# Optimization experiments

Hardware: AMD Instinct MI355X
Metric: run time of the kernel (lower is better)

The kernel has to match this reference:

```python
import jax, jax.numpy as jnp
import numpy as np

B, T, D, H, HD, L, V = 2048, 64, 128, 4, 32, 6, 256
DFF = 4 * D
PARAM_NAMES = ['tok_emb', 'pos_emb', 'Wq', 'Wk', 'Wv', 'Wo', 'bo', 'ln1_g', 'ln1_b',
               'W1', 'b1', 'W2', 'b2', 'ln2_g', 'ln2_b', 'lnf_g', 'lnf_b', 'Wh', 'bh']


def setup_inputs() -> dict:
    key = jax.random.key(0)
    ks = jax.random.split(key, 12)
    def n(k, shape, s=0.02):
        return jax.random.normal(k, shape, jnp.float32) * s
    return dict(
        idx=jax.random.randint(ks[0], (B, T), 0, V),
        tok_emb=n(ks[1], (V, D)),
        pos_emb=n(ks[2], (T, D)),
        Wq=n(ks[3], (L, H, D, HD)),
        Wk=n(ks[4], (L, H, D, HD)),
        Wv=n(ks[5], (L, H, D, HD)),
        Wo=n(ks[6], (L, D, D)), bo=jnp.zeros((L, D), jnp.float32),
        ln1_g=jnp.ones((L, D), jnp.float32), ln1_b=jnp.zeros((L, D), jnp.float32),
        W1=n(ks[7], (L, D, DFF)), b1=jnp.zeros((L, DFF), jnp.float32),
        W2=n(ks[8], (L, DFF, D)), b2=jnp.zeros((L, D), jnp.float32),
        ln2_g=jnp.ones((L, D), jnp.float32), ln2_b=jnp.zeros((L, D), jnp.float32),
        lnf_g=jnp.ones((D,), jnp.float32), lnf_b=jnp.zeros((D,), jnp.float32),
        Wh=n(ks[9], (D, V)), bh=jnp.zeros((V,), jnp.float32),
    )


def _ln(x, g, b):
    m = x.mean(-1, keepdims=True)
    v = x.var(-1, keepdims=True)  # biased, matches torch LayerNorm
    return (x - m) / jnp.sqrt(v + 1e-5) * g + b


def _forward(idx, p):
    x = p['tok_emb'][idx] + p['pos_emb'][None, :, :]  # [B,T,D]
    mask = jnp.tril(jnp.ones((T, T), bool))

    def block(x, lp):
        Wq, Wk, Wv, Wo, bo, g1, bb1, W1, b1, W2, b2, g2, bb2 = lp
        h = _ln(x, g1, bb1)
        q = jnp.einsum('btd,hde->bhte', h, Wq)
        k = jnp.einsum('btd,hde->bhte', h, Wk)
        v = jnp.einsum('btd,hde->bhte', h, Wv)
        s = jnp.einsum('bhte,bhse->bhts', q, k) * (HD ** -0.5)
        s = jnp.where(mask, s, -jnp.inf)
        w = jax.nn.softmax(s, axis=-1)  # dropout inactive (eval mode)
        o = jnp.einsum('bhts,bhse->bthe', w, v).reshape(B, T, D)  # concat heads
        x = x + o @ Wo + bo
        h2 = _ln(x, g2, bb2)
        x = x + jax.nn.relu(h2 @ W1 + b1) @ W2 + b2
        return x, None

    lp = (p['Wq'], p['Wk'], p['Wv'], p['Wo'], p['bo'], p['ln1_g'], p['ln1_b'],
          p['W1'], p['b1'], p['W2'], p['b2'], p['ln2_g'], p['ln2_b'])
    x, _ = jax.lax.scan(block, x, lp)
    x = _ln(x, p['lnf_g'], p['lnf_b'])
    return x @ p['Wh'] + p['bh']  # [B,T,V] logits


def reference(idx, tok_emb, pos_emb, Wq, Wk, Wv, Wo, bo, ln1_g, ln1_b,
              W1, b1, W2, b2, ln2_g, ln2_b, lnf_g, lnf_b, Wh, bh):
    p = dict(zip(PARAM_NAMES, (tok_emb, pos_emb, Wq, Wk, Wv, Wo, bo, ln1_g, ln1_b,
                               W1, b1, W2, b2, ln2_g, ln2_b, lnf_g, lnf_b, Wh, bh)))
    return _forward(idx, p)
```

## Files before the change

kernel.cpp:

```cpp
#include <hip/hip_runtime.h>

typedef unsigned short ushort_t;
typedef __attribute__((ext_vector_type(8))) short short8;
typedef __attribute__((ext_vector_type(4))) float float4_;

#define B_   2048
#define T_   64
#define D_   128
#define H_   4
#define HD_  32
#define L_   6
#define V_   256
#define DFF_ 512
#define BT_  (B_*T_)

static __device__ __forceinline__ float b2f(ushort_t u) {
    return __uint_as_float(((unsigned int)u) << 16);
}
static __device__ __forceinline__ ushort_t f2b(float f) {
    unsigned int x = __float_as_uint(f);
    return (ushort_t)((x + 0x7fffu + ((x >> 16) & 1u)) >> 16);
}
static __device__ __forceinline__ int bf16_mode(const ushort_t* flag_src) {
    return flag_src[0] == 0x3F80;
}

#define AS1C(p) ((const __attribute__((address_space(1))) void*)(p))
#define AS3(p)  ((__attribute__((address_space(3))) void*)(p))

#define NCVT 19
struct Cvt {
    const void* src[NCVT];
    long base[NCVT];
    long total;
};

__global__ __launch_bounds__(256) void convert_all(
    Cvt c, ushort_t* __restrict__ dst, const ushort_t* __restrict__ flag_src)
{
    long i = (long)blockIdx.x * 256 + threadIdx.x;
    if (i >= c.total) return;
    int s = 0;
    #pragma unroll 1
    while (s + 1 < NCVT && i >= c.base[s + 1]) s++;
    long j = i - c.base[s];
    if (bf16_mode(flag_src))
        dst[i] = ((const ushort_t*)c.src[s])[j];
    else
        dst[i] = f2b(((const float*)c.src[s])[j]);
}

__global__ __launch_bounds__(256) void repack_qkv(
    const ushort_t* __restrict__ Wq, const ushort_t* __restrict__ Wk,
    const ushort_t* __restrict__ Wv, ushort_t* __restrict__ outw)
{
    int i = blockIdx.x * 256 + threadIdx.x;
    int d = i & 127;
    int c = (i >> 7) % 384;
    int l = i / (384 * 128);
    int sel = c >> 7, hh = (c >> 5) & 3, e = c & 31;
    const ushort_t* W = (sel == 0) ? Wq : (sel == 1) ? Wk : Wv;
    outw[i] = W[((l * 4 + hh) * 128 + d) * 32 + e];
}

__global__ __launch_bounds__(256) void transpose_w(
    const ushort_t* __restrict__ in, ushort_t* __restrict__ out, int K, int N)
{
    long i = (long)blockIdx.x * 256 + threadIdx.x;
    int n = (int)(i % N);
    int k = (int)((i / N) % K);
    int l = (int)(i / ((long)N * K));
    out[((long)l * N + n) * K + k] = in[i];
}

__global__ __launch_bounds__(256) void embed_ln_kernel(
    const int* __restrict__ idx, const ushort_t* __restrict__ tok,
    const ushort_t* __restrict__ pos, const ushort_t* __restrict__ g,
    const ushort_t* __restrict__ bta, float* __restrict__ x,
    ushort_t* __restrict__ hout)
{
    int row  = blockIdx.x * 4 + (threadIdx.x >> 6);
    int lane = threadIdx.x & 63;
    int t = row & 63;
    int id = idx[row];
    float v0 = b2f(tok[id * 128 + lane])      + b2f(pos[t * 128 + lane]);
    float v1 = b2f(tok[id * 128 + lane + 64]) + b2f(pos[t * 128 + lane + 64]);
    long o = (long)row * 128 + lane;
    x[o] = v0; x[o + 64] = v1;
    float s  = v0 + v1;
    float sq = v0 * v0 + v1 * v1;
    #pragma unroll
    for (int off = 1; off < 64; off <<= 1) {
        s  += __shfl_xor(s,  off);
        sq += __shfl_xor(sq, off);
    }
    float mean = s * (1.0f / 128.0f);
    float var  = sq * (1.0f / 128.0f) - mean * mean;
    float rstd = rsqrtf(var + 1e-5f);
    hout[o]      = f2b((v0 - mean) * rstd * b2f(g[lane])      + b2f(bta[lane]));
    hout[o + 64] = f2b((v1 - mean) * rstd * b2f(g[lane + 64]) + b2f(bta[lane + 64]));
}

__global__ __launch_bounds__(256) void gemm_bt(
    const ushort_t* __restrict__ A, const ushort_t* __restrict__ Bt,
    const ushort_t* __restrict__ bias, void* __restrict__ outp,
    const ushort_t* __restrict__ flag, int M, int N, int K, int relu)
{
    __shared__ __align__(16) ushort_t As[128 * 64];
    __shared__ __align__(16) ushort_t Bs[128 * 64];
    const int tid  = threadIdx.x;
    const int wave = tid >> 6, lane = tid & 63;
    const int wm = wave >> 1, wn = wave & 1;
    const int row0 = blockIdx.x * 128, col0 = blockIdx.y * 128;

    float4_ acc[4][4];
    #pragma unroll
    for (int m = 0; m < 4; m++)
        #pragma unroll
        for (int n = 0; n < 4; n++) acc[m][n] = (float4_)0.0f;

    const int srow = lane >> 3;
    const int scg  = (lane & 7) ^ srow;
    const int fr = lane & 15, fq = lane >> 4;

    for (int k0 = 0; k0 < K; k0 += 64) {
        __syncthreads();
        #pragma unroll
        for (int i = 0; i < 4; i++) {
            int chunk = wave * 4 + i;
            int r = chunk * 8 + srow;
            __builtin_amdgcn_global_load_lds(
                AS1C(&A[(size_t)(row0 + r) * K + k0 + scg * 8]),
                AS3(&As[chunk * 512]), 16, 0, 0);
            __builtin_amdgcn_global_load_lds(
                AS1C(&Bt[(size_t)(col0 + r) * K + k0 + scg * 8]),
                AS3(&Bs[chunk * 512]), 16, 0, 0);
        }
        __syncthreads();

        #pragma unroll
        for (int ks = 0; ks < 2; ks++) {
            short8 af[4], bf[4];
            #pragma unroll
            for (int mt = 0; mt < 4; mt++) {
                int r = wm * 64 + mt * 16 + fr;
                af[mt] = *(const short8*)&As[r * 64 + (((ks * 4 + fq) ^ (r & 7)) * 8)];
            }
            #pragma unroll
            for (int nt = 0; nt < 4; nt++) {
                int r = wn * 64 + nt * 16 + fr;
                bf[nt] = *(const short8*)&Bs[r * 64 + (((ks * 4 + fq) ^ (r & 7)) * 8)];
            }
            #pragma unroll
            for (int mt = 0; mt < 4; mt++)
                #pragma unroll
                for (int nt = 0; nt < 4; nt++)
                    acc[mt][nt] = __builtin_amdgcn_mfma_f32_16x16x32_bf16(
                        af[mt], bf[nt], acc[mt][nt], 0, 0, 0);
        }
    }

    const int out_bf16 = (flag == nullptr) || bf16_mode(flag);
    #pragma unroll
    for (int nt = 0; nt < 4; nt++) {
        int gcol = col0 + wn * 64 + nt * 16 + fr;
        float bb = bias ? b2f(bias[gcol]) : 0.0f;
        #pragma unroll
        for (int mt = 0; mt < 4; mt++) {
            #pragma unroll
            for (int i = 0; i < 4; i++) {
                int grow = row0 + wm * 64 + mt * 16 + fq * 4 + i;
                float v = acc[mt][nt][i] + bb;
                if (relu) v = fmaxf(v, 0.0f);
                long off = (long)grow * N + gcol;
                if (out_bf16) ((ushort_t*)outp)[off] = f2b(v);
                else          ((float*)outp)[off] = v;
            }
        }
    }
}

__global__ __launch_bounds__(256) void gemm_ln(
    const ushort_t* __restrict__ A, const ushort_t* __restrict__ Bt,
    const ushort_t* __restrict__ bias, float* __restrict__ x,
    const ushort_t* __restrict__ g, const ushort_t* __restrict__ bta,
    ushort_t* __restrict__ hout, int M, int K)
{
    __shared__ __align__(16) ushort_t As[128 * 64];
    __shared__ __align__(16) ushort_t Bs[128 * 64];
    __shared__ float stats[128][2][2];
    const int tid  = threadIdx.x;
    const int wave = tid >> 6, lane = tid & 63;
    const int wm = wave >> 1, wn = wave & 1;
    const int row0 = blockIdx.x * 128;
    const int N = 128;

    float4_ acc[4][4];
    #pragma unroll
    for (int m = 0; m < 4; m++)
        #pragma unroll
        for (int n = 0; n < 4; n++) acc[m][n] = (float4_)0.0f;

    const int srow = lane >> 3;
    const int scg  = (lane & 7) ^ srow;
    const int fr = lane & 15, fq = lane >> 4;

    for (int k0 = 0; k0 < K; k0 += 64) {
        __syncthreads();
        #pragma unroll
        for (int i = 0; i < 4; i++) {
            int chunk = wave * 4 + i;
            int r = chunk * 8 + srow;
            __builtin_amdgcn_global_load_lds(
                AS1C(&A[(size_t)(row0 + r) * K + k0 + scg * 8]),
                AS3(&As[chunk * 512]), 16, 0, 0);
            __builtin_amdgcn_global_load_lds(
                AS1C(&Bt[(size_t)r * K + k0 + scg * 8]),
                AS3(&Bs[chunk * 512]), 16, 0, 0);
        }
        __syncthreads();

        #pragma unroll
        for (int ks = 0; ks < 2; ks++) {
            short8 af[4], bf[4];
            #pragma unroll
            for (int mt = 0; mt < 4; mt++) {
                int r = wm * 64 + mt * 16 + fr;
                af[mt] = *(const short8*)&As[r * 64 + (((ks * 4 + fq) ^ (r & 7)) * 8)];
            }
            #pragma unroll
            for (int nt = 0; nt < 4; nt++) {
                int r = wn * 64 + nt * 16 + fr;
                bf[nt] = *(const short8*)&Bs[r * 64 + (((ks * 4 + fq) ^ (r & 7)) * 8)];
            }
            #pragma unroll
            for (int mt = 0; mt < 4; mt++)
                #pragma unroll
                for (int nt = 0; nt < 4; nt++)
                    acc[mt][nt] = __builtin_amdgcn_mfma_f32_16x16x32_bf16(
                        af[mt], bf[nt], acc[mt][nt], 0, 0, 0);
        }
    }

    int   col[4];
    float bbias[4], gg[4], bln[4];
    #pragma unroll
    for (int nt = 0; nt < 4; nt++) {
        col[nt]  = wn * 64 + nt * 16 + fr;
        bbias[nt] = b2f(bias[col[nt]]);
        gg[nt]    = b2f(g[col[nt]]);
        bln[nt]   = b2f(bta[col[nt]]);
    }
    #pragma unroll
    for (int mt = 0; mt < 4; mt++) {
        #pragma unroll
        for (int i = 0; i < 4; i++) {
            int lr = wm * 64 + mt * 16 + fq * 4 + i;
            long rbase = (long)(row0 + lr) * N;
            float s = 0.0f, sq = 0.0f;
            #pragma unroll
            for (int nt = 0; nt < 4; nt++) {
                float nx = x[rbase + col[nt]] + acc[mt][nt][i] + bbias[nt];
                x[rbase + col[nt]] = nx;
                acc[mt][nt][i] = nx;
                s += nx; sq += nx * nx;
            }
            s  += __shfl_xor(s, 1);  sq += __shfl_xor(sq, 1);
            s  += __shfl_xor(s, 2);  sq += __shfl_xor(sq, 2);
            s  += __shfl_xor(s, 4);  sq += __shfl_xor(sq, 4);
            s  += __shfl_xor(s, 8);  sq += __shfl_xor(sq, 8);
            if (fr == 0) { stats[lr][wn][0] = s; stats[lr][wn][1] = sq; }
        }
    }
    __syncthreads();
    #pragma unroll
    for (int mt = 0; mt < 4; mt++) {
        #pragma unroll
        for (int i = 0; i < 4; i++) {
            int lr = wm * 64 + mt * 16 + fq * 4 + i;
            float s  = stats[lr][0][0] + stats[lr][1][0];
            float sq = stats[lr][0][1] + stats[lr][1][1];
            float mean = s * (1.0f / 128.0f);
            float var  = sq * (1.0f / 128.0f) - mean * mean;
            float rstd = rsqrtf(var + 1e-5f);
            long rbase = (long)(row0 + lr) * N;
            #pragma unroll
            for (int nt = 0; nt < 4; nt++) {
                float nx = acc[mt][nt][i];
                hout[rbase + col[nt]] = f2b((nx - mean) * rstd * gg[nt] + bln[nt]);
            }
        }
    }
}

__global__ __launch_bounds__(256) void attn_kernel(
    const ushort_t* __restrict__ qkv,
    ushort_t* __restrict__ out)
{
    __shared__ __align__(16) ushort_t Qs[64][40];
    __shared__ __align__(16) ushort_t Ks[64][40];
    __shared__ __align__(16) ushort_t Vt[32][72];
    __shared__ __align__(16) ushort_t Pb[64][72];
    const int tid = threadIdx.x;
    const int b = blockIdx.x >> 2, h = blockIdx.x & 3;
    const long base = (long)b * T_ * 384 + h * 32;

    {
        int t = tid >> 2, e8 = (tid & 3) * 8;
        const ushort_t* p = &qkv[base + (long)t * 384 + e8];
        short8 qv = *(const short8*)(p);
        short8 kv = *(const short8*)(p + 128);
        short8 vv = *(const short8*)(p + 256);
        *(short8*)&Qs[t][e8] = qv;
        *(short8*)&Ks[t][e8] = kv;
        #pragma unroll
        for (int j = 0; j < 8; j++) Vt[e8 + j][t] = (ushort_t)vv[j];
    }
    __syncthreads();

    const int w = tid >> 6, lane = tid & 63, fr = lane & 15, fq = lane >> 4;

    short8 qf = *(const short8*)&Qs[w * 16 + fr][fq * 8];
    float4_ s[4];
    #pragma unroll
    for (int tj = 0; tj < 4; tj++) s[tj] = (float4_)0.0f;
    #pragma unroll
    for (int tj = 0; tj < 4; tj++) {
        if (tj <= w) {
            short8 kf = *(const short8*)&Ks[tj * 16 + fr][fq * 8];
            s[tj] = __builtin_amdgcn_mfma_f32_16x16x32_bf16(qf, kf, s[tj], 0, 0, 0);
        }
    }

    const float scale = 0.17677669529663687f;
    float pv[4][4];
    #pragma unroll
    for (int i = 0; i < 4; i++) {
        float mx = -1.0e30f;
        float vv4[4];
        int   ok[4];
        #pragma unroll
        for (int tj = 0; tj < 4; tj++) {
            ok[tj] = (tj < w) || (tj == w && fr <= fq * 4 + i);
            float v = ok[tj] ? s[tj][i] * scale : -1.0e30f;
            vv4[tj] = v;
            mx = fmaxf(mx, v);
        }
        mx = fmaxf(mx, __shfl_xor(mx, 1));
        mx = fmaxf(mx, __shfl_xor(mx, 2));
        mx = fmaxf(mx, __shfl_xor(mx, 4));
        mx = fmaxf(mx, __shfl_xor(mx, 8));
        float sm = 0.0f;
        #pragma unroll
        for (int tj = 0; tj < 4; tj++) {
            float e = ok[tj] ? __expf(vv4[tj] - mx) : 0.0f;
            vv4[tj] = e;
            sm += e;
        }
        sm += __shfl_xor(sm, 1);
        sm += __shfl_xor(sm, 2);
        sm += __shfl_xor(sm, 4);
        sm += __shfl_xor(sm, 8);
        float inv = 1.0f / sm;
        #pragma unroll
        for (int tj = 0; tj < 4; tj++) pv[i][tj] = vv4[tj] * inv;
    }
    #pragma unroll
    for (int tj = 0; tj < 4; tj++)
        #pragma unroll
        for (int i = 0; i < 4; i++)
            Pb[w * 16 + fq * 4 + i][tj * 16 + fr] = f2b(pv[i][tj]);
    __syncthreads();

    float4_ o[2];
    o[0] = (float4_)0.0f; o[1] = (float4_)0.0f;
    #pragma unroll
    for (int ks = 0; ks < 2; ks++) {
        short8 pf = *(const short8*)&Pb[w * 16 + fr][ks * 32 + fq * 8];
        #pragma unroll
        for (int nt = 0; nt < 2; nt++) {
            short8 vf = *(const short8*)&Vt[nt * 16 + fr][ks * 32 + fq * 8];
            o[nt] = __builtin_amdgcn_mfma_f32_16x16x32_bf16(pf, vf, o[nt], 0, 0, 0);
        }
    }
    #pragma unroll
    for (int nt = 0; nt < 2; nt++)
        #pragma unroll
        for (int i = 0; i < 4; i++)
            out[(long)(b * T_ + w * 16 + fq * 4 + i) * 128 + h * 32 + nt * 16 + fr]
                = f2b(o[nt][i]);
}

extern "C" void kernel_launch(void* const* d_in, const int* in_sizes, int n_in,
                              void* d_out, int out_size, void* d_ws, size_t ws_size,
                              hipStream_t stream)
{
    (void)in_sizes; (void)n_in; (void)out_size; (void)ws_size;
    const int* idx = (const int*)d_in[0];
    const ushort_t* flag = (const ushort_t*)d_in[8];

    char* ws = (char*)d_ws;
    float*    x    = (float*)ws;     ws += (size_t)BT_ * D_ * 4;
    ushort_t* h    = (ushort_t*)ws;  ws += (size_t)BT_ * D_ * 2;
    ushort_t* qkvb = (ushort_t*)ws;  ws += (size_t)BT_ * 384 * 2;
    ushort_t* ao   = (ushort_t*)ws;  ws += (size_t)BT_ * D_ * 2;
    ushort_t* mid  = qkvb;
    ushort_t* wqkv = (ushort_t*)ws;  ws += (size_t)L_ * 384 * 128 * 2;
    ushort_t* wo   = (ushort_t*)ws;  ws += (size_t)L_ * 128 * 128 * 2;
    ushort_t* w1   = (ushort_t*)ws;  ws += (size_t)L_ * 512 * 128 * 2;
    ushort_t* w2   = (ushort_t*)ws;  ws += (size_t)L_ * 128 * 512 * 2;
    ushort_t* wh   = (ushort_t*)ws;  ws += (size_t)256 * 128 * 2;
    ushort_t* cvt  = (ushort_t*)ws;

    static const long cnt[NCVT] = {
        (long)V_*D_, (long)T_*D_,
        (long)L_*H_*D_*HD_, (long)L_*H_*D_*HD_, (long)L_*H_*D_*HD_,
        (long)L_*D_*D_, (long)L_*D_,
        (long)L_*D_, (long)L_*D_,
        (long)L_*D_*DFF_, (long)L_*DFF_,
        (long)L_*DFF_*D_, (long)L_*D_,
        (long)L_*D_, (long)L_*D_,
        (long)D_, (long)D_,
        (long)D_*V_, (long)V_
    };
    Cvt c;
    long off = 0;
    for (int i = 0; i < NCVT; i++) { c.src[i] = d_in[i + 1]; c.base[i] = off; off += cnt[i]; }
    c.total = off;
    ushort_t* ctok  = cvt + c.base[0];
    ushort_t* cpos  = cvt + c.base[1];
    ushort_t* cWq   = cvt + c.base[2];
    ushort_t* cWk   = cvt + c.base[3];
    ushort_t* cWv   = cvt + c.base[4];
    ushort_t* cWo   = cvt + c.base[5];
    ushort_t* cbo   = cvt + c.base[6];
    ushort_t* cln1g = cvt + c.base[7];
    ushort_t* cln1b = cvt + c.base[8];
    ushort_t* cW1   = cvt + c.base[9];
    ushort_t* cb1   = cvt + c.base[10];
    ushort_t* cW2   = cvt + c.base[11];
    ushort_t* cb2   = cvt + c.base[12];
    ushort_t* cln2g = cvt + c.base[13];
    ushort_t* cln2b = cvt + c.base[14];
    ushort_t* clnfg = cvt + c.base[15];
    ushort_t* clnfb = cvt + c.base[16];
    ushort_t* cWh   = cvt + c.base[17];
    ushort_t* cbh   = cvt + c.base[18];

    convert_all<<<(int)((c.total + 255) / 256), 256, 0, stream>>>(c, cvt, flag);

    repack_qkv <<<1152, 256, 0, stream>>>(cWq, cWk, cWv, wqkv);
    transpose_w<<<384,  256, 0, stream>>>(cWo, wo, 128, 128);
    transpose_w<<<1536, 256, 0, stream>>>(cW1, w1, 128, 512);
    transpose_w<<<1536, 256, 0, stream>>>(cW2, w2, 512, 128);
    transpose_w<<<128,  256, 0, stream>>>(cWh, wh, 128, 256);
    embed_ln_kernel<<<BT_ / 4, 256, 0, stream>>>(idx, ctok, cpos, cln1g, cln1b, x, h);

    for (int l = 0; l < L_; l++) {
        gemm_bt<<<dim3(BT_ / 128, 3), 256, 0, stream>>>(
            h, wqkv + l * 384 * 128, nullptr, qkvb, nullptr, BT_, 384, 128, 0);
        attn_kernel<<<B_ * H_, 256, 0, stream>>>(qkvb, ao);
        gemm_ln<<<BT_ / 128, 256, 0, stream>>>(
            ao, wo + l * 128 * 128, cbo + l * 128, x,
            cln2g + l * 128, cln2b + l * 128, h, BT_, 128);
        gemm_bt<<<dim3(BT_ / 128, 4), 256, 0, stream>>>(
            h, w1 + l * 512 * 128, cb1 + l * 512, mid, nullptr, BT_, 512, 128, 1);
        const ushort_t* ng = (l < L_ - 1) ? (cln1g + (l + 1) * 128) : clnfg;
        const ushort_t* nb = (l < L_ - 1) ? (cln1b + (l + 1) * 128) : clnfb;
        gemm_ln<<<BT_ / 128, 256, 0, stream>>>(
            mid, w2 + l * 128 * 512, cb2 + l * 128, x, ng, nb, h, BT_, 512);
    }
    gemm_bt<<<dim3(BT_ / 128, 2), 256, 0, stream>>>(
        h, wh, cbh, d_out, flag, BT_, 256, 128, 0);
}
```

Measured before the change: 1.689 ms.

## Fuse FFN up-projection, ReLU and down-projection into one kernel

```diff
diff --git a/kernel.cpp b/kernel.cpp
--- a/kernel.cpp
+++ b/kernel.cpp
@@ -293,6 +293,195 @@
     }
 }
 
+__global__ __launch_bounds__(256) void ffn_fused(
+    const ushort_t* __restrict__ hin,
+    const ushort_t* __restrict__ w1,
+    const ushort_t* __restrict__ b1v,
+    const ushort_t* __restrict__ w2,
+    const ushort_t* __restrict__ b2v,
+    float* __restrict__ x,
+    const ushort_t* __restrict__ g, const ushort_t* __restrict__ bta,
+    ushort_t* __restrict__ hout)
+{
+    __shared__ __align__(16) ushort_t Hs[128 * 128];
+    __shared__ __align__(16) ushort_t Ms[128 * 128];
+    __shared__ __align__(16) ushort_t Bs[128 * 64];
+    const int tid  = threadIdx.x;
+    const int wave = tid >> 6, lane = tid & 63;
+    const int wm = wave >> 1, wn = wave & 1;
+    const int row0 = blockIdx.x * 128;
+
+    const int srow = lane >> 3;
+    const int scg  = (lane & 7) ^ srow;
+    const int fr = lane & 15, fq = lane >> 4;
+
+    {
+        int lr4 = lane >> 4, pg = lane & 15;
+        #pragma unroll
+        for (int i = 0; i < 8; i++) {
+            int c = wave * 8 + i;
+            int r = c * 4 + lr4;
+            int kg = pg ^ (r & 7);
+            __builtin_amdgcn_global_load_lds(
+                AS1C(&hin[(size_t)(row0 + r) * 128 + kg * 8]),
+                AS3(&Hs[c * 512]), 16, 0, 0);
+        }
+    }
+
+    float4_ acc2[4][4];
+    #pragma unroll
+    for (int m = 0; m < 4; m++)
+        #pragma unroll
+        for (int n = 0; n < 4; n++) acc2[m][n] = (float4_)0.0f;
+
+    #pragma unroll 1
+    for (int c = 0; c < 4; c++) {
+        const ushort_t* Wc = w1 + (size_t)c * 128 * 128;
+        float4_ acc1[4][4];
+        #pragma unroll
+        for (int m = 0; m < 4; m++)
+            #pragma unroll
+            for (int n = 0; n < 4; n++) acc1[m][n] = (float4_)0.0f;
+
+        #pragma unroll 1
+        for (int k0 = 0; k0 < 128; k0 += 64) {
+            __syncthreads();
+            #pragma unroll
+            for (int i = 0; i < 4; i++) {
+                int chunk = wave * 4 + i;
+                int r = chunk * 8 + srow;
+                __builtin_amdgcn_global_load_lds(
+                    AS1C(&Wc[(size_t)r * 128 + k0 + scg * 8]),
+                    AS3(&Bs[chunk * 512]), 16, 0, 0);
+            }
+            __syncthreads();
+            #pragma unroll
+            for (int ks = 0; ks < 2; ks++) {
+                int kb = (k0 >> 5) + ks;
+                short8 af[4], bf[4];
+                #pragma unroll
+                for (int mt = 0; mt < 4; mt++) {
+                    int r = wm * 64 + mt * 16 + fr;
+                    af[mt] = *(const short8*)&Hs[r * 128 + (((kb * 4 + fq) ^ (r & 7)) * 8)];
+                }
+                #pragma unroll
+                for (int nt = 0; nt < 4; nt++) {
+                    int r = wn * 64 + nt * 16 + fr;
+                    bf[nt] = *(const short8*)&Bs[r * 64 + (((ks * 4 + fq) ^ (r & 7)) * 8)];
+                }
+                #pragma unroll
+                for (int mt = 0; mt < 4; mt++)
+                    #pragma unroll
+                    for (int nt = 0; nt < 4; nt++)
+                        acc1[mt][nt] = __builtin_amdgcn_mfma_f32_16x16x32_bf16(
+                            af[mt], bf[nt], acc1[mt][nt], 0, 0, 0);
+            }
+        }
+
+        #pragma unroll
+        for (int nt = 0; nt < 4; nt++) {
+            int col = wn * 64 + nt * 16 + fr;
+            float bb = b2f(b1v[c * 128 + col]);
+            #pragma unroll
+            for (int mt = 0; mt < 4; mt++) {
+                #pragma unroll
+                for (int i = 0; i < 4; i++) {
+                    int row = wm * 64 + mt * 16 + fq * 4 + i;
+                    float v = fmaxf(acc1[mt][nt][i] + bb, 0.0f);
+                    Ms[row * 128 + (((col >> 3) ^ (row & 7)) * 8) + (col & 7)] = f2b(v);
+                }
+            }
+        }
+
+        #pragma unroll 1
+        for (int k0 = 0; k0 < 128; k0 += 64) {
+            __syncthreads();
+            #pragma unroll
+            for (int i = 0; i < 4; i++) {
+                int chunk = wave * 4 + i;
+                int r = chunk * 8 + srow;
+                __builtin_amdgcn_global_load_lds(
+                    AS1C(&w2[(size_t)r * 512 + c * 128 + k0 + scg * 8]),
+                    AS3(&Bs[chunk * 512]), 16, 0, 0);
+            }
+            __syncthreads();
+            #pragma unroll
+            for (int ks = 0; ks < 2; ks++) {
+                int kb = (k0 >> 5) + ks;
+                short8 af[4], bf[4];
+                #pragma unroll
+                for (int mt = 0; mt < 4; mt++) {
+                    int r = wm * 64 + mt * 16 + fr;
+                    af[mt] = *(const short8*)&Ms[r * 128 + (((kb * 4 + fq) ^ (r & 7)) * 8)];
+                }
+                #pragma unroll
+                for (int nt = 0; nt < 4; nt++) {
+                    int r = wn * 64 + nt * 16 + fr;
+                    bf[nt] = *(const short8*)&Bs[r * 64 + (((ks * 4 + fq) ^ (r & 7)) * 8)];
+                }
+                #pragma unroll
+                for (int mt = 0; mt < 4; mt++)
+                    #pragma unroll
+                    for (int nt = 0; nt < 4; nt++)
+                        acc2[mt][nt] = __builtin_amdgcn_mfma_f32_16x16x32_bf16(
+                            af[mt], bf[nt], acc2[mt][nt], 0, 0, 0);
+            }
+        }
+    }
+
+    __syncthreads();
+    float (*stats)[2][2] = (float (*)[2][2])(void*)Bs;
+    int   col[4];
+    float bbias[4], gg[4], bln[4];
+    #pragma unroll
+    for (int nt = 0; nt < 4; nt++) {
+        col[nt]  = wn * 64 + nt * 16 + fr;
+        bbias[nt] = b2f(b2v[col[nt]]);
+        gg[nt]    = b2f(g[col[nt]]);
+        bln[nt]   = b2f(bta[col[nt]]);
+    }
+    #pragma unroll
+    for (int mt = 0; mt < 4; mt++) {
+        #pragma unroll
+        for (int i = 0; i < 4; i++) {
+            int lr = wm * 64 + mt * 16 + fq * 4 + i;
+            long rbase = (long)(row0 + lr) * 128;
+            float s = 0.0f, sq = 0.0f;
+            #pragma unroll
+            for (int nt = 0; nt < 4; nt++) {
+                float nx = x[rbase + col[nt]] + acc2[mt][nt][i] + bbias[nt];
+                x[rbase + col[nt]] = nx;
+                acc2[mt][nt][i] = nx;
+                s += nx; sq += nx * nx;
+            }
+            s  += __shfl_xor(s, 1);  sq += __shfl_xor(sq, 1);
+            s  += __shfl_xor(s, 2);  sq += __shfl_xor(sq, 2);
+            s  += __shfl_xor(s, 4);  sq += __shfl_xor(sq, 4);
+            s  += __shfl_xor(s, 8);  sq += __shfl_xor(sq, 8);
+            if (fr == 0) { stats[lr][wn][0] = s; stats[lr][wn][1] = sq; }
+        }
+    }
+    __syncthreads();
+    #pragma unroll
+    for (int mt = 0; mt < 4; mt++) {
+        #pragma unroll
+        for (int i = 0; i < 4; i++) {
+            int lr = wm * 64 + mt * 16 + fq * 4 + i;
+            float s  = stats[lr][0][0] + stats[lr][1][0];
+            float sq = stats[lr][0][1] + stats[lr][1][1];
+            float mean = s * (1.0f / 128.0f);
+            float var  = sq * (1.0f / 128.0f) - mean * mean;
+            float rstd = rsqrtf(var + 1e-5f);
+            long rbase = (long)(row0 + lr) * 128;
+            #pragma unroll
+            for (int nt = 0; nt < 4; nt++) {
+                float nx = acc2[mt][nt][i];
+                hout[rbase + col[nt]] = f2b((nx - mean) * rstd * gg[nt] + bln[nt]);
+            }
+        }
+    }
+}
+
 __global__ __launch_bounds__(256) void attn_kernel(
     const ushort_t* __restrict__ qkv,
     ushort_t* __restrict__ out)
@@ -404,7 +593,6 @@
     ushort_t* h    = (ushort_t*)ws;  ws += (size_t)BT_ * D_ * 2;
     ushort_t* qkvb = (ushort_t*)ws;  ws += (size_t)BT_ * 384 * 2;
     ushort_t* ao   = (ushort_t*)ws;  ws += (size_t)BT_ * D_ * 2;
-    ushort_t* mid  = qkvb;
     ushort_t* wqkv = (ushort_t*)ws;  ws += (size_t)L_ * 384 * 128 * 2;
     ushort_t* wo   = (ushort_t*)ws;  ws += (size_t)L_ * 128 * 128 * 2;
     ushort_t* w1   = (ushort_t*)ws;  ws += (size_t)L_ * 512 * 128 * 2;
@@ -463,12 +651,11 @@
         gemm_ln<<<BT_ / 128, 256, 0, stream>>>(
             ao, wo + l * 128 * 128, cbo + l * 128, x,
             cln2g + l * 128, cln2b + l * 128, h, BT_, 128);
-        gemm_bt<<<dim3(BT_ / 128, 4), 256, 0, stream>>>(
-            h, w1 + l * 512 * 128, cb1 + l * 512, mid, nullptr, BT_, 512, 128, 1);
         const ushort_t* ng = (l < L_ - 1) ? (cln1g + (l + 1) * 128) : clnfg;
         const ushort_t* nb = (l < L_ - 1) ? (cln1b + (l + 1) * 128) : clnfb;
-        gemm_ln<<<BT_ / 128, 256, 0, stream>>>(
-            mid, w2 + l * 128 * 512, cb2 + l * 128, x, ng, nb, h, BT_, 512);
+        ffn_fused<<<BT_ / 128, 256, 0, stream>>>(
+            h, w1 + l * 512 * 128, cb1 + l * 512,
+            w2 + l * 128 * 512, cb2 + l * 128, x, ng, nb, h);
     }
     gemm_bt<<<dim3(BT_ / 128, 2), 256, 0, stream>>>(
         h, wh, cbh, d_out, flag, BT_, 256, 128, 0);
```

New measurement: 1.675 ms. About the same (-0.8%).
